# Kernel optimization log

Measured on AMD Instinct MI355X. Metric: run time of the kernel, lower is better.

## Reference

```python
import jax, jax.numpy as jnp
import numpy as np

B, N, D = 16, 1024, 768
H = 12
DK = 768  # projection_dim_keys
DV = 768  # projection_dim_values
EK = DK // H
EV = DV // H


def setup_inputs() -> dict:
    key = jax.random.key(0)
    ks = jax.random.split(key, 7)
    s = 0.02
    return {
        "x": jax.random.normal(ks[0], (B, N, D), dtype=jnp.float32),
        "Wqk_w": jax.random.normal(ks[1], (2 * DK, D), dtype=jnp.float32) * s,
        "Wqk_b": jax.random.normal(ks[2], (2 * DK,), dtype=jnp.float32) * s,
        "Wv_w": jax.random.normal(ks[3], (DV, D), dtype=jnp.float32) * s,
        "Wv_b": jax.random.normal(ks[4], (DV,), dtype=jnp.float32) * s,
        "Wo_w": jax.random.normal(ks[5], (D, DV), dtype=jnp.float32) * s,
        "Wo_b": jax.random.normal(ks[6], (D,), dtype=jnp.float32) * s,
    }


def reference(x, Wqk_w, Wqk_b, Wv_w, Wv_b, Wo_w, Wo_b):
    b, n, _ = x.shape
    # fused Q/K projection: (b, n, 2*DK)
    qk = x @ Wqk_w.T + Wqk_b
    # rearrange 'b n (h e qk) -> qk b h n e' (last axis decomposes as (h, e, 2))
    qk = qk.reshape(b, n, H, EK, 2)
    queries = jnp.transpose(qk[..., 0], (0, 2, 1, 3))  # (b, h, n, e)
    keys = jnp.transpose(qk[..., 1], (0, 2, 1, 3))     # (b, h, n, e)
    # V projection: 'b n (h e k) -> k b h n e' with k=1
    v = (x @ Wv_w.T + Wv_b).reshape(b, n, H, EV)
    values = jnp.transpose(v, (0, 2, 1, 3))            # (b, h, n, ev)
    scores = jnp.einsum('bhqd,bhkd->bhqk', queries, keys)
    scale = jnp.asarray(DK ** 0.5, dtype=x.dtype)
    # NOTE: original code applies softmax FIRST, then divides by sqrt(dk)
    attn = jax.nn.softmax(scores, axis=-1) / scale
    # dropout prob = 0.0 (eval) -> identity
    out = jnp.einsum('bhsl,bhlv->bhsv', attn, values)  # (b, h, n, ev)
    concat = jnp.transpose(out, (0, 2, 1, 3)).reshape(b, n, H * EV)
    return concat @ Wo_w.T + Wo_b
```

## Files before the change

### kernel.cpp

```cpp
#include <hip/hip_runtime.h>
#include <hip/hip_bf16.h>


typedef __attribute__((ext_vector_type(4))) float    f32x4;
typedef __attribute__((ext_vector_type(8))) short    s16x8;
typedef __attribute__((ext_vector_type(4))) short    s16x4;
typedef __attribute__((ext_vector_type(4))) unsigned u32x4;
typedef __attribute__((ext_vector_type(2))) unsigned u32x2;

static __device__ __forceinline__ short f2bf(float f) {
  unsigned u = __builtin_bit_cast(unsigned, f);
  u += 0x7fff + ((u >> 16) & 1);
  return (short)(u >> 16);
}

static __device__ __forceinline__ unsigned cvt_pk_bf16(float lo, float hi) {
  unsigned r;
  asm("v_cvt_pk_bf16_f32 %0, %1, %2" : "=v"(r) : "v"(lo), "v"(hi));
  return r;
}

static __device__ __forceinline__ void gload16(const void* g, void* l) {
  __builtin_amdgcn_global_load_lds(
      (const __attribute__((address_space(1))) void*)g,
      (__attribute__((address_space(3))) void*)l, 16, 0, 0);
}

__global__ void cvt_x_kernel(const float* __restrict__ x, short* __restrict__ xb, int n4) {
  int stride = gridDim.x * blockDim.x;
  for (int t = blockIdx.x * blockDim.x + threadIdx.x; t < n4; t += stride) {
    f32x4 v = *(const f32x4*)(x + 4 * (size_t)t);
    s16x4 o;
#pragma unroll
    for (int i = 0; i < 4; ++i) o[i] = f2bf(v[i]);
    *(s16x4*)(xb + 4 * (size_t)t) = o;
  }
}

__global__ void pack_w_kernel(const float* __restrict__ Wqk, const float* __restrict__ qkb,
                              const float* __restrict__ Wv,  const float* __restrict__ vb,
                              const float* __restrict__ Wo,  const float* __restrict__ ob,
                              short* __restrict__ Wall, float* __restrict__ ball) {
  int stride = gridDim.x * blockDim.x;
  for (int t = blockIdx.x * blockDim.x + threadIdx.x; t < 3072 * 768; t += stride) {
    int j = t / 768, k = t - j * 768;
    float v;
    if (j < 768)        v = Wqk[(((j   >> 6) << 7) + ((j    & 63) << 1) + 0) * 768 + k];
    else if (j < 1536)  { int jj = j -  768; v = Wqk[(((jj >> 6) << 7) + ((jj & 63) << 1) + 1) * 768 + k]; }
    else if (j < 2304)  { int jj = j - 1536; v = Wv[jj * 768 + k]; }
    else                { int jj = j - 2304; v = Wo[jj * 768 + k]; }
    Wall[t] = f2bf(v);
  }
  for (int t = blockIdx.x * blockDim.x + threadIdx.x; t < 3072; t += stride) {
    float v;
    if (t < 768)        v = qkb[((t >> 6) << 7) + ((t & 63) << 1)];
    else if (t < 1536)  { int jj = t -  768; v = qkb[((jj >> 6) << 7) + ((jj & 63) << 1) + 1]; }
    else if (t < 2304)  v = vb[t - 1536];
    else                v = ob[t - 2304];
    ball[t] = v;
  }
}

template <int MODE>
__global__ __launch_bounds__(256)
void gemm_bt(const short* __restrict__ A, const short* __restrict__ Bw,
             const float* __restrict__ bias,
             short* __restrict__ Qo, short* __restrict__ Ko, short* __restrict__ Vo,
             float* __restrict__ Fo) {
  __shared__ short As[2][128 * 32];
  __shared__ short Bs[2][128 * 32];
  const int tid = threadIdx.x;
  const int lane = tid & 63, wid = tid >> 6;
  const int wr = wid >> 1, wc = wid & 1;
  const int lrow = lane & 15, lk = lane >> 4;
  int lin = blockIdx.y * gridDim.x + blockIdx.x;
  const int cpx = (gridDim.x * gridDim.y) >> 3;
  lin = (lin & 7) * cpx + (lin >> 3);
  const int n0 = (lin % gridDim.x) * 128;
  const int m0 = (lin / gridDim.x) * 128;
  const int r2 = tid >> 2, c2 = (tid & 3) * 8;

  f32x4 acc[4][4] = {};

  {
    const short* ga = A  + (size_t)(m0 + r2) * 768 + c2;
    const short* gb = Bw + (size_t)(n0 + r2) * 768 + c2;
    gload16(ga,            &As[0][tid * 8]);
    gload16(ga + 64 * 768, &As[0][(256 + tid) * 8]);
    gload16(gb,            &Bs[0][tid * 8]);
    gload16(gb + 64 * 768, &Bs[0][(256 + tid) * 8]);
  }

  for (int kt = 0; kt < 24; ++kt) {
    __syncthreads();
    const int cur = kt & 1;
    if (kt + 1 < 24) {
      const int nxt = cur ^ 1;
      const short* ga = A  + (size_t)(m0 + r2) * 768 + (kt + 1) * 32 + c2;
      const short* gb = Bw + (size_t)(n0 + r2) * 768 + (kt + 1) * 32 + c2;
      gload16(ga,            &As[nxt][tid * 8]);
      gload16(ga + 64 * 768, &As[nxt][(256 + tid) * 8]);
      gload16(gb,            &Bs[nxt][tid * 8]);
      gload16(gb + 64 * 768, &Bs[nxt][(256 + tid) * 8]);
    }
    s16x8 a[4], b[4];
#pragma unroll
    for (int mf = 0; mf < 4; ++mf)
      a[mf] = *(const s16x8*)&As[cur][(wr * 64 + mf * 16 + lrow) * 32 + lk * 8];
#pragma unroll
    for (int nf = 0; nf < 4; ++nf)
      b[nf] = *(const s16x8*)&Bs[cur][(wc * 64 + nf * 16 + lrow) * 32 + lk * 8];
#pragma unroll
    for (int mf = 0; mf < 4; ++mf)
#pragma unroll
      for (int nf = 0; nf < 4; ++nf)
        acc[mf][nf] = __builtin_amdgcn_mfma_f32_16x16x32_bf16(a[mf], b[nf], acc[mf][nf], 0, 0, 0);
  }

  const int g4 = lk * 4;
#pragma unroll
  for (int nf = 0; nf < 4; ++nf) {
    const int jc = n0 + wc * 64 + nf * 16 + lrow;
    const float bs = bias[jc];
#pragma unroll
    for (int mf = 0; mf < 4; ++mf) {
      f32x4 v = acc[mf][nf];
      const int mb = m0 + wr * 64 + mf * 16 + g4;
      if (MODE == 1) {
#pragma unroll
        for (int i = 0; i < 4; ++i)
          Fo[(size_t)(mb + i) * 768 + jc] = v[i] + bs;
      } else {
        const int bi = mb >> 10, n = mb & 1023;
        if (jc < 768) {
          const int h = jc >> 6, e = jc & 63;
          short* dst = Qo + (((size_t)bi * 12 + h) << 16) + (n << 6) + e;
#pragma unroll
          for (int i = 0; i < 4; ++i) dst[i << 6] = f2bf(v[i] + bs);
        } else if (jc < 1536) {
          const int jj = jc - 768;
          const int h = jj >> 6, e = jj & 63;
          short* dst = Ko + (((size_t)bi * 12 + h) << 16) + (n << 6) + e;
#pragma unroll
          for (int i = 0; i < 4; ++i) dst[i << 6] = f2bf(v[i] + bs);
        } else {
          const int jj = jc - 1536;
          const int h = jj >> 6, e = jj & 63;
          s16x4 pk;
#pragma unroll
          for (int i = 0; i < 4; ++i) pk[i] = f2bf(v[i] + bs);
          *(s16x4*)(Vo + (((size_t)bi * 12 + h) * 64 + e) * 1024 + n) = pk;
        }
      }
    }
  }
}

__global__ __launch_bounds__(256, 4)
void attn_kernel(const short* __restrict__ Q, const short* __restrict__ K,
                 const short* __restrict__ VT, short* __restrict__ Co) {
  __shared__ short Ks[2][4096];
  __shared__ short Vs[2][4096];
  const int tid = threadIdx.x, lane = tid & 63, wid = tid >> 6;
  const int lrow = lane & 15, lk = lane >> 4;
  const int bh = blockIdx.x, qt = blockIdx.y;
  const int bi = bh / 12, h = bh - bi * 12;
  const int q0 = qt * 128 + wid * 32;
  const size_t base = (size_t)bh << 16;

  const short* Kb = K  + base;
  const short* Vb = VT + base;

  const int sr = tid >> 3, sj = tid & 7;
  const int jsw = (sj ^ (sr & 7)) << 3;
  const short* ksrc0 = Kb + (size_t)sr * 64 + jsw;
  const short* vsrc0 = Vb + (size_t)sr * 1024 + jsw;

  const int rs = lrow & 7;
  const int ko0 = (lk ^ rs) << 3;
  const int ko1 = ((4 | lk) ^ rs) << 3;
  const int vhalf = (lk & 1) * 4;
  int vo[2][2];
#pragma unroll
  for (int kh = 0; kh < 2; ++kh) {
    const int g = kh * 4 + (lk >> 1);
    vo[kh][0] = ((g ^ rs) << 3) + vhalf;
    vo[kh][1] = (((g | 2) ^ rs) << 3) + vhalf;
  }

  s16x8 qf[2][2];
#pragma unroll
  for (int qi = 0; qi < 2; ++qi)
#pragma unroll
    for (int kk = 0; kk < 2; ++kk)
      qf[qi][kk] = *(const s16x8*)&Q[base + (size_t)(q0 + qi * 16 + lrow) * 64 + kk * 32 + lk * 8];

  f32x4 o[2][4] = {};
  float lr[2] = {0.f, 0.f};

  gload16(ksrc0,             &Ks[0][tid * 8]);
  gload16(ksrc0 + 32 * 64,   &Ks[0][(tid + 256) * 8]);
  gload16(vsrc0,             &Vs[0][tid * 8]);
  gload16(vsrc0 + 32 * 1024, &Vs[0][(tid + 256) * 8]);

  for (int t = 0; t < 16; ++t) {
    const int cur = t & 1;
    asm volatile("s_waitcnt vmcnt(0)" ::: "memory");
    __builtin_amdgcn_s_barrier();
    if (t < 15) {
      const int nxt = cur ^ 1;
      const int kvn = (t + 1) * 64;
      const short* ks = ksrc0 + (size_t)kvn * 64;
      const short* vs = vsrc0 + kvn;
      gload16(ks,             &Ks[nxt][tid * 8]);
      gload16(ks + 32 * 64,   &Ks[nxt][(tid + 256) * 8]);
      gload16(vs,             &Vs[nxt][tid * 8]);
      gload16(vs + 32 * 1024, &Vs[nxt][(tid + 256) * 8]);
    }

    f32x4 s[2][4] = {};
    __builtin_amdgcn_s_setprio(1);
#pragma unroll
    for (int kvf = 0; kvf < 4; ++kvf) {
      const short* krow = &Ks[cur][(kvf * 16 + lrow) * 64];
      s16x8 ka0 = *(const s16x8*)&krow[ko0];
      s16x8 ka1 = *(const s16x8*)&krow[ko1];
#pragma unroll
      for (int qi = 0; qi < 2; ++qi) {
        s[qi][kvf] = __builtin_amdgcn_mfma_f32_16x16x32_bf16(ka0, qf[qi][0], s[qi][kvf], 0, 0, 0);
        s[qi][kvf] = __builtin_amdgcn_mfma_f32_16x16x32_bf16(ka1, qf[qi][1], s[qi][kvf], 0, 0, 0);
      }
    }
    __builtin_amdgcn_s_setprio(0);

#pragma unroll
    for (int qi = 0; qi < 2; ++qi) {
      float acc = 0.f;
#pragma unroll
      for (int kvf = 0; kvf < 4; ++kvf)
#pragma unroll
        for (int i = 0; i < 4; ++i) {
          float p = __expf(s[qi][kvf][i] - 16.f);
          s[qi][kvf][i] = p;
          acc += p;
        }
      lr[qi] += acc;
    }

    s16x8 pf[2][2];
#pragma unroll
    for (int qi = 0; qi < 2; ++qi)
#pragma unroll
      for (int kh = 0; kh < 2; ++kh) {
        u32x4 pw;
        pw[0] = cvt_pk_bf16(s[qi][2 * kh][0],     s[qi][2 * kh][1]);
        pw[1] = cvt_pk_bf16(s[qi][2 * kh][2],     s[qi][2 * kh][3]);
        pw[2] = cvt_pk_bf16(s[qi][2 * kh + 1][0], s[qi][2 * kh + 1][1]);
        pw[3] = cvt_pk_bf16(s[qi][2 * kh + 1][2], s[qi][2 * kh + 1][3]);
        pf[qi][kh] = __builtin_bit_cast(s16x8, pw);
      }

    __builtin_amdgcn_s_setprio(1);
#pragma unroll
    for (int ef = 0; ef < 4; ++ef) {
      const short* vrow = &Vs[cur][(ef * 16 + lrow) * 64];
#pragma unroll
      for (int kh = 0; kh < 2; ++kh) {
        s16x4 v0 = *(const s16x4*)&vrow[vo[kh][0]];
        s16x4 v1 = *(const s16x4*)&vrow[vo[kh][1]];
        s16x8 va = __builtin_shufflevector(v0, v1, 0, 1, 2, 3, 4, 5, 6, 7);
#pragma unroll
        for (int qi = 0; qi < 2; ++qi)
          o[qi][ef] = __builtin_amdgcn_mfma_f32_16x16x32_bf16(va, pf[qi][kh], o[qi][ef], 0, 0, 0);
      }
    }
    __builtin_amdgcn_s_setprio(0);
  }

#pragma unroll
  for (int qi = 0; qi < 2; ++qi) {
    lr[qi] += __shfl_xor(lr[qi], 16, 64);
    lr[qi] += __shfl_xor(lr[qi], 32, 64);
  }

  const float isq = 0.03608439182435161f;
#pragma unroll
  for (int qi = 0; qi < 2; ++qi) {
    const float inv = isq / lr[qi];
    const int q = q0 + qi * 16 + lrow;
    short* dst = Co + ((size_t)(bi * 1024 + q)) * 768 + h * 64;
#pragma unroll
    for (int ef = 0; ef < 4; ++ef) {
      u32x2 pk2;
      pk2[0] = cvt_pk_bf16(o[qi][ef][0] * inv, o[qi][ef][1] * inv);
      pk2[1] = cvt_pk_bf16(o[qi][ef][2] * inv, o[qi][ef][3] * inv);
      *(s16x4*)(dst + ef * 16 + lk * 4) = __builtin_bit_cast(s16x4, pk2);
    }
  }
}

extern "C" void kernel_launch(void* const* d_in, const int* in_sizes, int n_in,
                              void* d_out, int out_size, void* d_ws, size_t ws_size,
                              hipStream_t stream) {
  const float* x     = (const float*)d_in[0];
  const float* Wqk_w = (const float*)d_in[1];
  const float* Wqk_b = (const float*)d_in[2];
  const float* Wv_w  = (const float*)d_in[3];
  const float* Wv_b  = (const float*)d_in[4];
  const float* Wo_w  = (const float*)d_in[5];
  const float* Wo_b  = (const float*)d_in[6];
  float* out = (float*)d_out;

  char* w = (char*)d_ws;
  short* xb   = (short*)(w);
  short* Wall = (short*)(w + 25165824);
  float* ball = (float*)(w + 29884416);
  short* Qb   = (short*)(w + 29896704);
  short* Kb   = (short*)(w + 55062528);
  short* VTb  = (short*)(w + 80228352);
  short* Co   = xb;

  cvt_x_kernel<<<2048, 256, 0, stream>>>(x, xb, 16384 * 768 / 4);
  pack_w_kernel<<<1024, 256, 0, stream>>>(Wqk_w, Wqk_b, Wv_w, Wv_b, Wo_w, Wo_b, Wall, ball);
  gemm_bt<0><<<dim3(18, 128), 256, 0, stream>>>(xb, Wall, ball, Qb, Kb, VTb, nullptr);
  attn_kernel<<<dim3(192, 8), 256, 0, stream>>>(Qb, Kb, VTb, Co);
  gemm_bt<1><<<dim3(6, 128), 256, 0, stream>>>(Co, Wall + 2304 * 768, ball + 2304,
                                               nullptr, nullptr, nullptr, out);
}
```

Before: 299.9 us.

## Triple-buffer GEMM LDS with swizzle, setprio, and LDS-staged vectorized epilogue

Reworks the projection GEMM to use a 3-stage LDS ring with prefetch distance two and explicit vmcnt waits instead of a full __syncthreads per k-step. It applies an XOR swizzle to LDS columns to cut bank conflicts, and raises wave priority around the MFMA block. The epilogue now stages accumulator tiles through LDS so Q/K and the fp32 output are written with wide coalesced stores rather than scattered 2-byte or 4-byte stores. The extra LDS stage raises shared memory per block, which may lower occupancy.

Result: no change. 295.5 us (-1.5%).

```diff
diff --git a/kernel.cpp b/kernel.cpp
--- a/kernel.cpp
+++ b/kernel.cpp
@@ -67,8 +67,7 @@
              const float* __restrict__ bias,
              short* __restrict__ Qo, short* __restrict__ Ko, short* __restrict__ Vo,
              float* __restrict__ Fo) {
-  __shared__ short As[2][128 * 32];
-  __shared__ short Bs[2][128 * 32];
+  __shared__ short Ls[6][4096];
   const int tid = threadIdx.x;
   const int lane = tid & 63, wid = tid >> 6;
   const int wr = wid >> 1, wc = wid & 1;
@@ -78,78 +77,113 @@
   lin = (lin & 7) * cpx + (lin >> 3);
   const int n0 = (lin % gridDim.x) * 128;
   const int m0 = (lin / gridDim.x) * 128;
-  const int r2 = tid >> 2, c2 = (tid & 3) * 8;
+
+  const int sr = tid >> 2;
+  const int swzc = ((tid & 3) ^ ((tid >> 3) & 3)) << 3;
+  const short* ga0 = A  + (size_t)(m0 + sr) * 768 + swzc;
+  const short* gb0 = Bw + (size_t)(n0 + sr) * 768 + swzc;
+  const int xoff = (lk ^ ((lrow >> 1) & 3)) << 3;
 
   f32x4 acc[4][4] = {};
 
-  {
-    const short* ga = A  + (size_t)(m0 + r2) * 768 + c2;
-    const short* gb = Bw + (size_t)(n0 + r2) * 768 + c2;
-    gload16(ga,            &As[0][tid * 8]);
-    gload16(ga + 64 * 768, &As[0][(256 + tid) * 8]);
-    gload16(gb,            &Bs[0][tid * 8]);
-    gload16(gb + 64 * 768, &Bs[0][(256 + tid) * 8]);
-  }
-
+#pragma unroll
+  for (int kk = 0; kk < 2; ++kk) {
+    const short* ga = ga0 + kk * 32;
+    const short* gb = gb0 + kk * 32;
+    gload16(ga,            &Ls[kk][tid * 8]);
+    gload16(ga + 64 * 768, &Ls[kk][(256 + tid) * 8]);
+    gload16(gb,            &Ls[3 + kk][tid * 8]);
+    gload16(gb + 64 * 768, &Ls[3 + kk][(256 + tid) * 8]);
+  }
+
+  int cb = 0, sb = 2;
   for (int kt = 0; kt < 24; ++kt) {
-    __syncthreads();
-    const int cur = kt & 1;
-    if (kt + 1 < 24) {
-      const int nxt = cur ^ 1;
-      const short* ga = A  + (size_t)(m0 + r2) * 768 + (kt + 1) * 32 + c2;
-      const short* gb = Bw + (size_t)(n0 + r2) * 768 + (kt + 1) * 32 + c2;
-      gload16(ga,            &As[nxt][tid * 8]);
-      gload16(ga + 64 * 768, &As[nxt][(256 + tid) * 8]);
-      gload16(gb,            &Bs[nxt][tid * 8]);
-      gload16(gb + 64 * 768, &Bs[nxt][(256 + tid) * 8]);
+    if (kt < 22) asm volatile("s_waitcnt vmcnt(4)" ::: "memory");
+    else         asm volatile("s_waitcnt vmcnt(0)" ::: "memory");
+    __builtin_amdgcn_s_barrier();
+    if (kt + 2 < 24) {
+      const short* ga = ga0 + (kt + 2) * 32;
+      const short* gb = gb0 + (kt + 2) * 32;
+      gload16(ga,            &Ls[sb][tid * 8]);
+      gload16(ga + 64 * 768, &Ls[sb][(256 + tid) * 8]);
+      gload16(gb,            &Ls[3 + sb][tid * 8]);
+      gload16(gb + 64 * 768, &Ls[3 + sb][(256 + tid) * 8]);
     }
     s16x8 a[4], b[4];
 #pragma unroll
     for (int mf = 0; mf < 4; ++mf)
-      a[mf] = *(const s16x8*)&As[cur][(wr * 64 + mf * 16 + lrow) * 32 + lk * 8];
+      a[mf] = *(const s16x8*)&Ls[cb][(wr * 64 + mf * 16 + lrow) * 32 + xoff];
 #pragma unroll
     for (int nf = 0; nf < 4; ++nf)
-      b[nf] = *(const s16x8*)&Bs[cur][(wc * 64 + nf * 16 + lrow) * 32 + lk * 8];
+      b[nf] = *(const s16x8*)&Ls[3 + cb][(wc * 64 + nf * 16 + lrow) * 32 + xoff];
+    __builtin_amdgcn_s_setprio(1);
 #pragma unroll
     for (int mf = 0; mf < 4; ++mf)
 #pragma unroll
       for (int nf = 0; nf < 4; ++nf)
         acc[mf][nf] = __builtin_amdgcn_mfma_f32_16x16x32_bf16(a[mf], b[nf], acc[mf][nf], 0, 0, 0);
-  }
-
+    __builtin_amdgcn_s_setprio(0);
+    cb = (cb == 2) ? 0 : cb + 1;
+    sb = (sb == 2) ? 0 : sb + 1;
+  }
+
+  __syncthreads();
+  float* tw = (float*)((char*)&Ls[0][0] + wid * 4352);
+  const int creg = n0 + wc * 64;
   const int g4 = lk * 4;
-#pragma unroll
-  for (int nf = 0; nf < 4; ++nf) {
-    const int jc = n0 + wc * 64 + nf * 16 + lrow;
-    const float bs = bias[jc];
+
+  if (MODE == 0 && creg >= 1536) {
+    const int h = (creg - 1536) >> 6;
+#pragma unroll
+    for (int nf = 0; nf < 4; ++nf) {
+      const int e = nf * 16 + lrow;
+      const float bs = bias[creg + e];
+#pragma unroll
+      for (int mf = 0; mf < 4; ++mf) {
+        f32x4 v = acc[mf][nf];
+        const int mb = m0 + wr * 64 + mf * 16 + g4;
+        const int bi = mb >> 10, n = mb & 1023;
+        s16x4 pk;
+#pragma unroll
+        for (int i = 0; i < 4; ++i) pk[i] = f2bf(v[i] + bs);
+        *(s16x4*)(Vo + (((size_t)bi * 12 + h) * 64 + e) * 1024 + n) = pk;
+      }
+    }
+  } else {
 #pragma unroll
     for (int mf = 0; mf < 4; ++mf) {
-      f32x4 v = acc[mf][nf];
-      const int mb = m0 + wr * 64 + mf * 16 + g4;
-      if (MODE == 1) {
+#pragma unroll
+      for (int nf = 0; nf < 4; ++nf) {
+        const float bs = bias[creg + nf * 16 + lrow];
 #pragma unroll
         for (int i = 0; i < 4; ++i)
-          Fo[(size_t)(mb + i) * 768 + jc] = v[i] + bs;
+          tw[(g4 + i) * 68 + nf * 16 + lrow] = acc[mf][nf][i] + bs;
+      }
+      if (MODE == 0) {
+        const int hq = (creg >> 6) % 12;
+        short* dst0 = (creg < 768) ? Qo : Ko;
+#pragma unroll
+        for (int p = 0; p < 2; ++p) {
+          const int row = (lane >> 3) + p * 8, c8 = (lane & 7) * 8;
+          f32x4 v0 = *(const f32x4*)&tw[row * 68 + c8];
+          f32x4 v1 = *(const f32x4*)&tw[row * 68 + c8 + 4];
+          u32x4 pk;
+          pk[0] = cvt_pk_bf16(v0[0], v0[1]);
+          pk[1] = cvt_pk_bf16(v0[2], v0[3]);
+          pk[2] = cvt_pk_bf16(v1[0], v1[1]);
+          pk[3] = cvt_pk_bf16(v1[2], v1[3]);
+          const int m = m0 + wr * 64 + mf * 16 + row;
+          const int bi = m >> 10, n = m & 1023;
+          *(s16x8*)(dst0 + (((size_t)bi * 12 + hq) << 16) + ((size_t)n << 6) + c8) =
+              __builtin_bit_cast(s16x8, pk);
+        }
       } else {
-        const int bi = mb >> 10, n = mb & 1023;
-        if (jc < 768) {
-          const int h = jc >> 6, e = jc & 63;
-          short* dst = Qo + (((size_t)bi * 12 + h) << 16) + (n << 6) + e;
-#pragma unroll
-          for (int i = 0; i < 4; ++i) dst[i << 6] = f2bf(v[i] + bs);
-        } else if (jc < 1536) {
-          const int jj = jc - 768;
-          const int h = jj >> 6, e = jj & 63;
-          short* dst = Ko + (((size_t)bi * 12 + h) << 16) + (n << 6) + e;
-#pragma unroll
-          for (int i = 0; i < 4; ++i) dst[i << 6] = f2bf(v[i] + bs);
-        } else {
-          const int jj = jc - 1536;
-          const int h = jj >> 6, e = jj & 63;
-          s16x4 pk;
-#pragma unroll
-          for (int i = 0; i < 4; ++i) pk[i] = f2bf(v[i] + bs);
-          *(s16x4*)(Vo + (((size_t)bi * 12 + h) * 64 + e) * 1024 + n) = pk;
+#pragma unroll
+        for (int p = 0; p < 4; ++p) {
+          const int row = (lane >> 4) + p * 4, c4 = (lane & 15) * 4;
+          f32x4 v = *(const f32x4*)&tw[row * 68 + c4];
+          const int m = m0 + wr * 64 + mf * 16 + row;
+          *(f32x4*)&Fo[(size_t)m * 768 + creg + c4] = v;
         }
       }
     }
```
